# Kernel tuning notes

Measured on AMD Instinct MI355X. Metric: run time of the kernel, lower is better.

Reference implementation:

```python
import jax, jax.numpy as jnp
import numpy as np

B, N, DIM, HEADS, DIM_HEAD = 2, 2048, 1024, 16, 64
INNER = HEADS * DIM_HEAD
LN_EPS = 1e-5


def setup_inputs() -> dict:
    key = jax.random.key(0)
    k1, k2, k3 = jax.random.split(key, 3)
    x = jax.random.normal(k1, (B, N, DIM), dtype=jnp.float32)
    ln_w = jnp.ones((DIM,), dtype=jnp.float32)
    ln_b = jnp.zeros((DIM,), dtype=jnp.float32)
    w_qkv = jax.random.normal(k2, (DIM, 3 * INNER), dtype=jnp.float32) * (DIM ** -0.5)
    w_out = jax.random.normal(k3, (INNER, DIM), dtype=jnp.float32) * (INNER ** -0.5)
    return {"x": x, "ln_w": ln_w, "ln_b": ln_b, "w_qkv": w_qkv, "w_out": w_out}


def reference(x, ln_w, ln_b, w_qkv, w_out):
    scale = DIM_HEAD ** -0.5
    # LayerNorm over last dim
    mu = jnp.mean(x, axis=-1, keepdims=True)
    var = jnp.var(x, axis=-1, keepdims=True)
    xn = (x - mu) / jnp.sqrt(var + LN_EPS) * ln_w + ln_b
    # qkv projection, split, reshape to b h n d
    qkv = xn @ w_qkv  # [B, N, 3*INNER]
    q, k, v = jnp.split(qkv, 3, axis=-1)
    def to_heads(t):
        return t.reshape(B, N, HEADS, DIM_HEAD).transpose(0, 2, 1, 3)
    q, k, v = to_heads(q) * scale, to_heads(k), to_heads(v)
    # scores + causal mask (triu with offset 1 masked)
    sim = jnp.einsum('bhid,bhjd->bhij', q, k)  # [B, H, N, N]
    causal_mask = jnp.triu(jnp.ones((N, N), dtype=bool), k=1)
    sim = jnp.where(causal_mask, -jnp.finfo(sim.dtype).max, sim)
    attn = jax.nn.softmax(sim, axis=-1)
    out = jnp.einsum('bhij,bhjd->bhid', attn, v)  # [B, H, N, D]
    out = out.transpose(0, 2, 1, 3).reshape(B, N, INNER)
    return out @ w_out
```

## Files before the change

### kernel.cpp

```cpp
#include <hip/hip_runtime.h>
#include <stdint.h>

#define BATCH 2
#define NSEQ  2048
#define DIMC  1024
#define NHEAD 16
#define DHEAD 64
#define QKVN  3072
#define MROWS 4096

typedef __attribute__((ext_vector_type(8))) unsigned short u16x8;
typedef __attribute__((ext_vector_type(4))) unsigned short u16x4;
typedef __attribute__((ext_vector_type(8))) short          bf16x8;
typedef __attribute__((ext_vector_type(4))) float          f32x4;

#define F32_PROBE 0x3F800000u
#define QSCALE 0.18033688f

__device__ __forceinline__ float b2f(unsigned short u) {
  union { unsigned int i; float f; } c; c.i = ((unsigned int)u) << 16; return c.f;
}
__device__ __forceinline__ unsigned short f2b(float f) {
  unsigned int u = __float_as_uint(f);
  return (unsigned short)((u + 0x7fffu + ((u >> 16) & 1u)) >> 16);
}
__device__ __forceinline__ float fast_exp2(float x) {
  return __builtin_amdgcn_exp2f(x);
}
__device__ __forceinline__ void async16(const unsigned short* g, unsigned short* s) {
  __builtin_amdgcn_global_load_lds(
      (const __attribute__((address_space(1))) unsigned int*)g,
      (__attribute__((address_space(3))) unsigned int*)s, 16, 0, 0);
}

__device__ __forceinline__ void tr_tile(const void* __restrict__ in,
                                        unsigned short* __restrict__ out,
                                        int R, int C, int r0, int c0, bool f32,
                                        int t, unsigned short (*tile)[33],
                                        int scale_below) {
  int tx = t & 31, ty = t >> 5;
  float sc = (c0 < scale_below) ? QSCALE : 1.0f;
  if (f32) {
    #pragma unroll
    for (int i = 0; i < 32; i += 8)
      tile[ty + i][tx] = f2b(((const float*)in)[(size_t)(r0 + ty + i) * C + c0 + tx] * sc);
  } else {
    #pragma unroll
    for (int i = 0; i < 32; i += 8)
      tile[ty + i][tx] = f2b(b2f(((const unsigned short*)in)[(size_t)(r0 + ty + i) * C + c0 + tx]) * sc);
  }
  __syncthreads();
  #pragma unroll
  for (int i = 0; i < 32; i += 8)
    out[(size_t)(c0 + ty + i) * R + r0 + tx] = tile[tx][ty + i];
}

__global__ __launch_bounds__(256) void prep_kernel(const void* __restrict__ x,
                                                   const void* __restrict__ w,
                                                   const void* __restrict__ bb,
                                                   unsigned short* __restrict__ xn,
                                                   const void* __restrict__ w_qkv,
                                                   unsigned short* __restrict__ wqkvT,
                                                   const void* __restrict__ w_out,
                                                   unsigned short* __restrict__ woutT,
                                                   const unsigned int* __restrict__ probe) {
  __shared__ unsigned short tile[32][33];
  __shared__ float red[8];
  bool f32 = (*probe == F32_PROBE);
  int bid = blockIdx.x, t = threadIdx.x;

  if (bid < MROWS) {
    int row = bid;
    float v0, v1, v2, v3, w0, w1, w2, w3, bb0, bb1, bb2, bb3;
    if (f32) {
      const float* xr = (const float*)x + (size_t)row * DIMC;
      float4 xv = *(const float4*)(xr + t * 4);
      v0 = xv.x; v1 = xv.y; v2 = xv.z; v3 = xv.w;
      float4 wv = *(const float4*)((const float*)w + t * 4);
      w0 = wv.x; w1 = wv.y; w2 = wv.z; w3 = wv.w;
      float4 bv = *(const float4*)((const float*)bb + t * 4);
      bb0 = bv.x; bb1 = bv.y; bb2 = bv.z; bb3 = bv.w;
    } else {
      const unsigned short* xr = (const unsigned short*)x + (size_t)row * DIMC;
      u16x4 xv = *(const u16x4*)(xr + t * 4);
      v0 = b2f(xv[0]); v1 = b2f(xv[1]); v2 = b2f(xv[2]); v3 = b2f(xv[3]);
      u16x4 wv = *(const u16x4*)((const unsigned short*)w + t * 4);
      w0 = b2f(wv[0]); w1 = b2f(wv[1]); w2 = b2f(wv[2]); w3 = b2f(wv[3]);
      u16x4 bv = *(const u16x4*)((const unsigned short*)bb + t * 4);
      bb0 = b2f(bv[0]); bb1 = b2f(bv[1]); bb2 = b2f(bv[2]); bb3 = b2f(bv[3]);
    }
    float s = v0 + v1 + v2 + v3;
    float q = v0 * v0 + v1 * v1 + v2 * v2 + v3 * v3;
    #pragma unroll
    for (int off = 1; off < 64; off <<= 1) { s += __shfl_xor(s, off); q += __shfl_xor(q, off); }
    int wv_ = t >> 6;
    if ((t & 63) == 0) { red[wv_] = s; red[4 + wv_] = q; }
    __syncthreads();
    s = red[0] + red[1] + red[2] + red[3];
    q = red[4] + red[5] + red[6] + red[7];
    float mu  = s * (1.0f / DIMC);
    float var = q * (1.0f / DIMC) - mu * mu;
    float rstd = rsqrtf(var + 1e-5f);
    u16x4 o;
    o[0] = f2b((v0 - mu) * rstd * w0 + bb0);
    o[1] = f2b((v1 - mu) * rstd * w1 + bb1);
    o[2] = f2b((v2 - mu) * rstd * w2 + bb2);
    o[3] = f2b((v3 - mu) * rstd * w3 + bb3);
    *(u16x4*)(xn + (size_t)row * DIMC + t * 4) = o;
  } else if (bid < MROWS + 3072) {
    int tid = bid - MROWS;
    tr_tile(w_qkv, wqkvT, DIMC, QKVN, (tid / 96) * 32, (tid % 96) * 32, f32, t, tile, 1024);
  } else {
    int tid = bid - (MROWS + 3072);
    tr_tile(w_out, woutT, DIMC, DIMC, (tid >> 5) * 32, (tid & 31) * 32, f32, t, tile, 0);
  }
}

__global__ __launch_bounds__(256) void transpose_kernel(const void* __restrict__ in,
                                                        unsigned short* __restrict__ out,
                                                        int R, int C,
                                                        const unsigned int* __restrict__ probe) {
  __shared__ unsigned short tile[32][33];
  bool f32 = (*probe == F32_PROBE);
  int t = threadIdx.x;
  tr_tile(in, out, R, C, blockIdx.y * 32, blockIdx.x * 32, f32, t, tile, 0);
}

__global__ __launch_bounds__(256) void gemm_bt(const unsigned short* __restrict__ A,
                                               const unsigned short* __restrict__ Bt,
                                               void* __restrict__ Cv,
                                               int M, int N, int K, int lda,
                                               int detect_out,
                                               const unsigned int* __restrict__ probe,
                                               unsigned short* __restrict__ vt_out) {
  __shared__ unsigned short As[128 * 32];
  __shared__ unsigned short Bs[128 * 32];
  int t = threadIdx.x;
  int lane = t & 63, wave = t >> 6;
  int l16 = lane & 15, quad = lane >> 4;
  int wm = (wave & 1) * 64, wn = (wave >> 1) * 64;
  int bm = blockIdx.x * 128, bn = blockIdx.y * 128;

  f32x4 acc[4][4] = {};

  int srow = t >> 2;
  int scol = (t & 3) * 8;
  const unsigned short* Ap = A  + (size_t)(bm + srow) * lda + scol;
  const unsigned short* Bp = Bt + (size_t)(bn + srow) * K + scol;
  unsigned short* As0 = &As[srow * 32 + scol];
  unsigned short* As1 = &As[(64 + srow) * 32 + scol];
  unsigned short* Bs0 = &Bs[srow * 32 + scol];
  unsigned short* Bs1 = &Bs[(64 + srow) * 32 + scol];

  for (int k0 = 0; k0 < K; k0 += 32) {
    __syncthreads();
    async16(Ap + k0, As0);
    async16(Ap + (size_t)64 * lda + k0, As1);
    async16(Bp + k0, Bs0);
    async16(Bp + (size_t)64 * K + k0, Bs1);
    __syncthreads();
    bf16x8 af[4], bfr[4];
    #pragma unroll
    for (int mi = 0; mi < 4; mi++)
      af[mi] = *(const bf16x8*)&As[(wm + mi * 16 + l16) * 32 + quad * 8];
    #pragma unroll
    for (int ni = 0; ni < 4; ni++)
      bfr[ni] = *(const bf16x8*)&Bs[(wn + ni * 16 + l16) * 32 + quad * 8];
    #pragma unroll
    for (int mi = 0; mi < 4; mi++)
      #pragma unroll
      for (int ni = 0; ni < 4; ni++)
        acc[mi][ni] = __builtin_amdgcn_mfma_f32_16x16x32_bf16(af[mi], bfr[ni], acc[mi][ni], 0, 0, 0);
  }
  if (vt_out != nullptr && bn >= 2048) {
    #pragma unroll
    for (int mi = 0; mi < 4; mi++)
      #pragma unroll
      for (int ni = 0; ni < 4; ni++) {
        int gc = bn + wn + ni * 16 + l16;
        int hh = (gc >> 6) & 15;
        int dd = gc & 63;
        int gr0 = bm + wm + mi * 16 + quad * 4;
        int bb2 = gr0 >> 11;
        int n0  = gr0 & 2047;
        u16x4 pk;
        #pragma unroll
        for (int r = 0; r < 4; r++) pk[r] = f2b(acc[mi][ni][r]);
        *(u16x4*)&vt_out[(((size_t)(bb2 * 16 + hh) * 64 + dd) << 11) + n0] = pk;
      }
    return;
  }
  bool f32out = detect_out && (*probe == F32_PROBE);
  #pragma unroll
  for (int mi = 0; mi < 4; mi++)
    #pragma unroll
    for (int ni = 0; ni < 4; ni++)
      #pragma unroll
      for (int r = 0; r < 4; r++) {
        int gr = bm + wm + mi * 16 + quad * 4 + r;
        int gc = bn + wn + ni * 16 + l16;
        if (f32out) ((float*)Cv)[(size_t)gr * N + gc] = acc[mi][ni][r];
        else ((unsigned short*)Cv)[(size_t)gr * N + gc] = f2b(acc[mi][ni][r]);
      }
}

__global__ __launch_bounds__(256) void gemm_bt_n64(const unsigned short* __restrict__ A,
                                                   const unsigned short* __restrict__ Bt,
                                                   void* __restrict__ Cv,
                                                   int M, int N, int K, int lda,
                                                   int detect_out,
                                                   const unsigned int* __restrict__ probe) {
  __shared__ unsigned short As[128 * 32];
  __shared__ unsigned short Bs[64 * 32];
  int t = threadIdx.x;
  int lane = t & 63, wave = t >> 6;
  int l16 = lane & 15, quad = lane >> 4;
  int wm = (wave & 1) * 64, wn = (wave >> 1) * 32;
  int bm = blockIdx.x * 128, bn = blockIdx.y * 64;

  f32x4 acc[4][2] = {};

  int srow = t >> 2;
  int scol = (t & 3) * 8;
  const unsigned short* Ap = A  + (size_t)(bm + srow) * lda + scol;
  const unsigned short* Bp = Bt + (size_t)(bn + srow) * K + scol;
  unsigned short* As0 = &As[srow * 32 + scol];
  unsigned short* As1 = &As[(64 + srow) * 32 + scol];
  unsigned short* Bs0 = &Bs[srow * 32 + scol];

  for (int k0 = 0; k0 < K; k0 += 32) {
    __syncthreads();
    async16(Ap + k0, As0);
    async16(Ap + (size_t)64 * lda + k0, As1);
    async16(Bp + k0, Bs0);
    __syncthreads();
    bf16x8 af[4], bfr[2];
    #pragma unroll
    for (int mi = 0; mi < 4; mi++)
      af[mi] = *(const bf16x8*)&As[(wm + mi * 16 + l16) * 32 + quad * 8];
    #pragma unroll
    for (int ni = 0; ni < 2; ni++)
      bfr[ni] = *(const bf16x8*)&Bs[(wn + ni * 16 + l16) * 32 + quad * 8];
    #pragma unroll
    for (int mi = 0; mi < 4; mi++)
      #pragma unroll
      for (int ni = 0; ni < 2; ni++)
        acc[mi][ni] = __builtin_amdgcn_mfma_f32_16x16x32_bf16(af[mi], bfr[ni], acc[mi][ni], 0, 0, 0);
  }
  bool f32out = detect_out && (*probe == F32_PROBE);
  #pragma unroll
  for (int mi = 0; mi < 4; mi++)
    #pragma unroll
    for (int ni = 0; ni < 2; ni++)
      #pragma unroll
      for (int r = 0; r < 4; r++) {
        int gr = bm + wm + mi * 16 + quad * 4 + r;
        int gc = bn + wn + ni * 16 + l16;
        if (f32out) ((float*)Cv)[(size_t)gr * N + gc] = acc[mi][ni][r];
        else ((unsigned short*)Cv)[(size_t)gr * N + gc] = f2b(acc[mi][ni][r]);
      }
}

__device__ __forceinline__ int swz(int row, int chunk) {
  return row * 64 + ((chunk ^ (row & 7)) << 3);
}

__global__ __launch_bounds__(256) void attn_v4(unsigned short* __restrict__ qkv,
                                               const unsigned short* __restrict__ vt) {
  __shared__ unsigned short lds[20480];

  int t = threadIdx.x;
  int lane = t & 63, w = t >> 6;
  int l16 = lane & 15, quad = lane >> 4;
  int pair = blockIdx.x;
  int bh = blockIdx.y;
  int b = bh >> 4, h = bh & 15;
  unsigned short* qbase = qkv + (size_t)(b * NSEQ) * QKVN + h * DHEAD;
  const unsigned short* kbase = qbase + 1024;
  const unsigned short* vtb = vt + (size_t)bh * DHEAD * NSEQ;
  unsigned short* Ps = lds + 16384;

  int sr = t >> 3, sc = t & 7;

  for (int ph = 0; ph < 2; ph++) {
    int qt = ph ? pair : 31 - pair;
    int q0 = qt * 64;

    const unsigned short* qp = qbase + (size_t)(q0 + w * 16 + l16) * QKVN + quad * 8;
    bf16x8 bq0 = *(const bf16x8*)(qp);
    bf16x8 bq1 = *(const bf16x8*)(qp + 32);

    float l_i = 0.f;
    f32x4 o[4] = {};
    u16x8 k0r, k1r, v0r, v1r;

    if (ph) __syncthreads();

    k0r = *(const u16x8*)(kbase + (size_t)sr * QKVN + sc * 8);
    k1r = *(const u16x8*)(kbase + (size_t)(sr + 32) * QKVN + sc * 8);
    v0r = *(const u16x8*)(vtb + (size_t)sr * NSEQ + sc * 8);
    v1r = *(const u16x8*)(vtb + (size_t)(sr + 32) * NSEQ + sc * 8);
    *(u16x8*)&lds[swz(sr, sc)]             = k0r;
    *(u16x8*)&lds[swz(sr + 32, sc)]        = k1r;
    *(u16x8*)&lds[8192 + swz(sr, sc)]      = v0r;
    *(u16x8*)&lds[8192 + swz(sr + 32, sc)] = v1r;
    __syncthreads();

    for (int jt = 0; jt <= qt; jt++) {
      const unsigned short* Kc = lds + (jt & 1) * 4096;
      const unsigned short* Vc = lds + 8192 + (jt & 1) * 4096;

      if (jt < qt) {
        int j0n = (jt + 1) * 64;
        k0r = *(const u16x8*)(kbase + (size_t)(j0n + sr) * QKVN + sc * 8);
        k1r = *(const u16x8*)(kbase + (size_t)(j0n + sr + 32) * QKVN + sc * 8);
        v0r = *(const u16x8*)(vtb + (size_t)sr * NSEQ + j0n + sc * 8);
        v1r = *(const u16x8*)(vtb + (size_t)(sr + 32) * NSEQ + j0n + sc * 8);
      }

      f32x4 s[4];
      #pragma unroll
      for (int mj = 0; mj < 4; mj++)
        #pragma unroll
        for (int r = 0; r < 4; r++) s[mj][r] = -32.0f;
      #pragma unroll
      for (int mj = 0; mj < 4; mj++) {
        bf16x8 ak0 = *(const bf16x8*)&Kc[swz(mj * 16 + l16, quad)];
        s[mj] = __builtin_amdgcn_mfma_f32_16x16x32_bf16(ak0, bq0, s[mj], 0, 0, 0);
        bf16x8 ak1 = *(const bf16x8*)&Kc[swz(mj * 16 + l16, 4 + quad)];
        s[mj] = __builtin_amdgcn_mfma_f32_16x16x32_bf16(ak1, bq1, s[mj], 0, 0, 0);
      }

      if (jt == qt) {
        int il = w * 16 + l16;
        #pragma unroll
        for (int mj = 0; mj < 4; mj++)
          #pragma unroll
          for (int r = 0; r < 4; r++)
            if (mj * 16 + quad * 4 + r > il) s[mj][r] = -1e30f;
      }

      #pragma unroll
      for (int mj = 0; mj < 4; mj++) {
        u16x4 pk;
        #pragma unroll
        for (int r = 0; r < 4; r++) {
          float p = fast_exp2(s[mj][r]);
          l_i += p;
          pk[r] = f2b(p);
        }
        int ch = mj * 2 + (quad >> 1);
        *(u16x4*)&Ps[swz(w * 16 + l16, ch) + (quad & 1) * 4] = pk;
      }

      #pragma unroll
      for (int ks = 0; ks < 2; ks++) {
        bf16x8 ap = *(const bf16x8*)&Ps[swz(w * 16 + l16, ks * 4 + quad)];
        #pragma unroll
        for (int d = 0; d < 4; d++) {
          bf16x8 bv = *(const bf16x8*)&Vc[swz(d * 16 + l16, ks * 4 + quad)];
          o[d] = __builtin_amdgcn_mfma_f32_16x16x32_bf16(ap, bv, o[d], 0, 0, 0);
        }
      }

      if (jt < qt) {
        unsigned short* Kn = lds + ((jt + 1) & 1) * 4096;
        unsigned short* Vn = lds + 8192 + ((jt + 1) & 1) * 4096;
        *(u16x8*)&Kn[swz(sr, sc)]      = k0r;
        *(u16x8*)&Kn[swz(sr + 32, sc)] = k1r;
        *(u16x8*)&Vn[swz(sr, sc)]      = v0r;
        *(u16x8*)&Vn[swz(sr + 32, sc)] = v1r;
        __syncthreads();
      }
    }

    l_i += __shfl_xor(l_i, 16);
    l_i += __shfl_xor(l_i, 32);
    #pragma unroll
    for (int r = 0; r < 4; r++) {
      float lr = __shfl(l_i, (lane & 48) | (quad * 4 + r));
      float inv = 1.0f / lr;
      int row = q0 + w * 16 + quad * 4 + r;
      #pragma unroll
      for (int d = 0; d < 4; d++)
        qbase[(size_t)row * QKVN + d * 16 + l16] = f2b(o[d][r] * inv);
    }
  }
}

extern "C" void kernel_launch(void* const* d_in, const int* in_sizes, int n_in,
                              void* d_out, int out_size, void* d_ws, size_t ws_size,
                              hipStream_t stream) {
  const void* x     = d_in[0];
  const void* ln_w  = d_in[1];
  const void* ln_b  = d_in[2];
  const void* w_qkv = d_in[3];
  const void* w_out = d_in[4];
  const unsigned int* probe = (const unsigned int*)d_in[1];

  unsigned short* wqkvT = (unsigned short*)d_ws;
  unsigned short* qkv   = wqkvT + (size_t)QKVN * DIMC;
  unsigned short* xn    = (unsigned short*)d_out;
  size_t base_e  = (size_t)QKVN * DIMC + (size_t)MROWS * QKVN;
  size_t vt_e    = (size_t)BATCH * NHEAD * DHEAD * NSEQ;
  size_t wout_e  = (size_t)DIMC * DIMC;
  bool fit_vt  = ws_size >= (base_e + vt_e) * 2;
  bool fit_all = ws_size >= (base_e + vt_e + wout_e) * 2;
  unsigned short* vtp   = fit_vt ? qkv + (size_t)MROWS * QKVN
                                 : ((unsigned short*)d_out) + ((size_t)4 * 1024 * 1024);
  unsigned short* woutT = fit_all ? vtp + vt_e : wqkvT;

  int prep_blocks = MROWS + 3072 + (fit_all ? 1024 : 0);
  prep_kernel<<<prep_blocks, 256, 0, stream>>>(x, ln_w, ln_b, xn, w_qkv, wqkvT,
                                               w_out, fit_all ? woutT : nullptr, probe);
  gemm_bt<<<dim3(MROWS / 128, QKVN / 128), 256, 0, stream>>>(
      xn, wqkvT, qkv, MROWS, QKVN, DIMC, DIMC, 0, probe, vtp);
  if (!fit_all)
    transpose_kernel<<<dim3(DIMC / 32, DIMC / 32), 256, 0, stream>>>(w_out, woutT, DIMC, DIMC, probe);
  attn_v4<<<dim3(NSEQ / 128, BATCH * NHEAD), 256, 0, stream>>>(qkv, vtp);
  gemm_bt_n64<<<dim3(MROWS / 128, DIMC / 64), 256, 0, stream>>>(
      qkv, woutT, d_out, MROWS, DIMC, DIMC, QKVN, 1, probe);
}
```

Measured before the change: 186.6 us.

## Replace QKV GEMM with 256x256-tile, 8-wave double-buffered pipelined kernel

The generic 128x128 QKV projection GEMM is replaced by a specialised kernel with 256x256 tiles, 512 threads, and a K-step of 64. It double-buffers the tiles in 128KB of LDS, uses an XOR-swizzled layout to avoid bank conflicts, interleaves async global-to-LDS loads with MFMA quarters, raises wave priority around the MFMA blocks, and swizzles the block order for L2 locality. The aim is to hide memory latency and raise MFMA utilisation in the largest GEMM. In exchange it hardcodes the problem shape and depends on a fragile manual barrier and waitcnt schedule.

```diff
diff --git a/kernel.cpp b/kernel.cpp
--- a/kernel.cpp
+++ b/kernel.cpp
@@ -126,82 +126,137 @@
   tr_tile(in, out, R, C, blockIdx.y * 32, blockIdx.x * 32, f32, t, tile, 0);
 }
 
-__global__ __launch_bounds__(256) void gemm_bt(const unsigned short* __restrict__ A,
-                                               const unsigned short* __restrict__ Bt,
-                                               void* __restrict__ Cv,
-                                               int M, int N, int K, int lda,
-                                               int detect_out,
-                                               const unsigned int* __restrict__ probe,
-                                               unsigned short* __restrict__ vt_out) {
-  __shared__ unsigned short As[128 * 32];
-  __shared__ unsigned short Bs[128 * 32];
+__device__ __forceinline__ void ldA8(bf16x8 (&dst)[8], const unsigned short* base,
+                                     int off, int ch0, int ch1) {
+  #pragma unroll
+  for (int mi = 0; mi < 4; ++mi) {
+    dst[mi * 2 + 0] = *(const bf16x8*)&base[off + mi * 1024 + ch0];
+    dst[mi * 2 + 1] = *(const bf16x8*)&base[off + mi * 1024 + ch1];
+  }
+}
+__device__ __forceinline__ void ldB4(bf16x8 (&dst)[4], const unsigned short* base,
+                                     int off, int ch0, int ch1) {
+  #pragma unroll
+  for (int ni = 0; ni < 2; ++ni) {
+    dst[ni * 2 + 0] = *(const bf16x8*)&base[off + ni * 1024 + ch0];
+    dst[ni * 2 + 1] = *(const bf16x8*)&base[off + ni * 1024 + ch1];
+  }
+}
+__device__ __forceinline__ void mfma16q(f32x4 (&acc)[8][4], const bf16x8 (&a)[8],
+                                        const bf16x8 (&b)[4], int R, int C) {
+  #pragma unroll
+  for (int kh = 0; kh < 2; ++kh)
+    #pragma unroll
+    for (int mi = 0; mi < 4; ++mi)
+      #pragma unroll
+      for (int ni = 0; ni < 2; ++ni)
+        acc[R * 4 + mi][C * 2 + ni] = __builtin_amdgcn_mfma_f32_16x16x32_bf16(
+            a[mi * 2 + kh], b[ni * 2 + kh], acc[R * 4 + mi][C * 2 + ni], 0, 0, 0);
+}
+
+#define SB    asm volatile("s_barrier" ::: "memory")
+#define WVM4  asm volatile("s_waitcnt vmcnt(4)" ::: "memory")
+#define WLG0  asm volatile("s_waitcnt lgkmcnt(0)" ::: "memory")
+#define PRIO1 __builtin_amdgcn_s_setprio(1)
+#define PRIO0 __builtin_amdgcn_s_setprio(0)
+#define STG(gp, g, k0, sb) async16((gp) + (size_t)(g) * 65536 + (k0), (sb) + (g) * 4096 + t8)
+
+__global__ __launch_bounds__(512) void gemm1_8p(const unsigned short* __restrict__ A,
+                                                const unsigned short* __restrict__ Bt,
+                                                unsigned short* __restrict__ C,
+                                                unsigned short* __restrict__ vt_out) {
+  __shared__ unsigned short lds[65536];
+  unsigned short* A0b = lds;
+  unsigned short* B0b = lds + 16384;
+  unsigned short* A1b = lds + 32768;
+  unsigned short* B1b = lds + 49152;
+
   int t = threadIdx.x;
-  int lane = t & 63, wave = t >> 6;
+  int lane = t & 63, wv = t >> 6;
   int l16 = lane & 15, quad = lane >> 4;
-  int wm = (wave & 1) * 64, wn = (wave >> 1) * 64;
-  int bm = blockIdx.x * 128, bn = blockIdx.y * 128;
-
-  f32x4 acc[4][4] = {};
-
-  int srow = t >> 2;
-  int scol = (t & 3) * 8;
-  const unsigned short* Ap = A  + (size_t)(bm + srow) * lda + scol;
-  const unsigned short* Bp = Bt + (size_t)(bn + srow) * K + scol;
-  unsigned short* As0 = &As[srow * 32 + scol];
-  unsigned short* As1 = &As[(64 + srow) * 32 + scol];
-  unsigned short* Bs0 = &Bs[srow * 32 + scol];
-  unsigned short* Bs1 = &Bs[(64 + srow) * 32 + scol];
-
-  for (int k0 = 0; k0 < K; k0 += 32) {
-    __syncthreads();
-    async16(Ap + k0, As0);
-    async16(Ap + (size_t)64 * lda + k0, As1);
-    async16(Bp + k0, Bs0);
-    async16(Bp + (size_t)64 * K + k0, Bs1);
-    __syncthreads();
-    bf16x8 af[4], bfr[4];
-    #pragma unroll
-    for (int mi = 0; mi < 4; mi++)
-      af[mi] = *(const bf16x8*)&As[(wm + mi * 16 + l16) * 32 + quad * 8];
-    #pragma unroll
-    for (int ni = 0; ni < 4; ni++)
-      bfr[ni] = *(const bf16x8*)&Bs[(wn + ni * 16 + l16) * 32 + quad * 8];
-    #pragma unroll
-    for (int mi = 0; mi < 4; mi++)
-      #pragma unroll
-      for (int ni = 0; ni < 4; ni++)
-        acc[mi][ni] = __builtin_amdgcn_mfma_f32_16x16x32_bf16(af[mi], bfr[ni], acc[mi][ni], 0, 0, 0);
-  }
-  if (vt_out != nullptr && bn >= 2048) {
-    #pragma unroll
-    for (int mi = 0; mi < 4; mi++)
-      #pragma unroll
-      for (int ni = 0; ni < 4; ni++) {
-        int gc = bn + wn + ni * 16 + l16;
+  int wr = wv >> 2, wc = wv & 3;
+
+  int bid = blockIdx.x;
+  int swzid = (bid & 7) * 24 + (bid >> 3);
+  int bx = swzid / 12, by = swzid % 12;
+  int bm = bx * 256, bn = by * 256;
+
+  int rl = t >> 3;
+  int sc8 = (((t & 7) ^ (rl & 7)) << 3);
+  int t8 = t * 8;
+  const unsigned short* Ag = A  + (size_t)(bm + rl) * 1024 + sc8;
+  const unsigned short* Bg = Bt + (size_t)(bn + rl) * 1024 + sc8;
+
+  int aoff = (wr * 128 + l16) * 64;
+  int boff = (wc * 64 + l16) * 64;
+  int ch0 = ((quad ^ (l16 & 7)) << 3);
+  int ch1 = (((quad + 4) ^ (l16 & 7)) << 3);
+
+  f32x4 acc[8][4] = {};
+  bf16x8 ar0[8], ar1[8], bc0[4], bc1[4];
+
+  STG(Ag, 0, 0, A0b); STG(Ag, 1, 0, A0b); STG(Ag, 2, 0, A0b); STG(Ag, 3, 0, A0b);
+  STG(Bg, 0, 0, B0b); STG(Bg, 1, 0, B0b); STG(Bg, 2, 0, B0b); STG(Bg, 3, 0, B0b);
+  STG(Ag, 0, 64, A1b); STG(Ag, 1, 64, A1b); STG(Ag, 2, 64, A1b); STG(Ag, 3, 64, A1b);
+  WVM4;
+  SB;
+
+  for (int i = 0; i < 8; ++i) {
+    const int k_b1 = (2 * i + 1) * 64;
+    const int k_n0 = ((2 * i + 2) & 15) * 64;
+    const int k_n1 = ((2 * i + 3) & 15) * 64;
+
+    ldA8(ar0, A0b, aoff, ch0, ch1);
+    ldB4(bc0, B0b, boff, ch0, ch1);
+    STG(Bg, 0, k_b1, B1b); STG(Bg, 1, k_b1, B1b);
+    SB; WLG0; PRIO1; mfma16q(acc, ar0, bc0, 0, 0); PRIO0; SB;
+    ldA8(ar1, A0b, aoff + 4096, ch0, ch1);
+    STG(Bg, 2, k_b1, B1b); STG(Bg, 3, k_b1, B1b);
+    SB; WLG0; PRIO1; mfma16q(acc, ar1, bc0, 1, 0); PRIO0; SB;
+    ldB4(bc1, B0b, boff + 2048, ch0, ch1);
+    STG(Ag, 0, k_n0, A0b); STG(Ag, 1, k_n0, A0b);
+    SB; WLG0; PRIO1; mfma16q(acc, ar0, bc1, 0, 1); PRIO0; SB;
+    STG(Ag, 2, k_n0, A0b); STG(Ag, 3, k_n0, A0b);
+    WVM4;
+    SB; PRIO1; mfma16q(acc, ar1, bc1, 1, 1); PRIO0; SB;
+
+    ldA8(ar0, A1b, aoff, ch0, ch1);
+    ldB4(bc0, B1b, boff, ch0, ch1);
+    STG(Bg, 0, k_n0, B0b); STG(Bg, 1, k_n0, B0b);
+    SB; WLG0; PRIO1; mfma16q(acc, ar0, bc0, 0, 0); PRIO0; SB;
+    ldA8(ar1, A1b, aoff + 4096, ch0, ch1);
+    STG(Bg, 2, k_n0, B0b); STG(Bg, 3, k_n0, B0b);
+    SB; WLG0; PRIO1; mfma16q(acc, ar1, bc0, 1, 0); PRIO0; SB;
+    ldB4(bc1, B1b, boff + 2048, ch0, ch1);
+    STG(Ag, 0, k_n1, A1b); STG(Ag, 1, k_n1, A1b);
+    SB; WLG0; PRIO1; mfma16q(acc, ar0, bc1, 0, 1); PRIO0; SB;
+    STG(Ag, 2, k_n1, A1b); STG(Ag, 3, k_n1, A1b);
+    WVM4;
+    SB; PRIO1; mfma16q(acc, ar1, bc1, 1, 1); PRIO0; SB;
+  }
+
+  bool vblk = (bn >= 2048);
+  #pragma unroll
+  for (int rf = 0; rf < 8; ++rf)
+    #pragma unroll
+    for (int cf = 0; cf < 4; ++cf) {
+      int gr0 = bm + wr * 128 + rf * 16 + quad * 4;
+      int gc  = bn + wc * 64 + cf * 16 + l16;
+      if (vblk) {
         int hh = (gc >> 6) & 15;
         int dd = gc & 63;
-        int gr0 = bm + wm + mi * 16 + quad * 4;
         int bb2 = gr0 >> 11;
         int n0  = gr0 & 2047;
         u16x4 pk;
         #pragma unroll
-        for (int r = 0; r < 4; r++) pk[r] = f2b(acc[mi][ni][r]);
+        for (int r = 0; r < 4; r++) pk[r] = f2b(acc[rf][cf][r]);
         *(u16x4*)&vt_out[(((size_t)(bb2 * 16 + hh) * 64 + dd) << 11) + n0] = pk;
-      }
-    return;
-  }
-  bool f32out = detect_out && (*probe == F32_PROBE);
-  #pragma unroll
-  for (int mi = 0; mi < 4; mi++)
-    #pragma unroll
-    for (int ni = 0; ni < 4; ni++)
-      #pragma unroll
-      for (int r = 0; r < 4; r++) {
-        int gr = bm + wm + mi * 16 + quad * 4 + r;
-        int gc = bn + wn + ni * 16 + l16;
-        if (f32out) ((float*)Cv)[(size_t)gr * N + gc] = acc[mi][ni][r];
-        else ((unsigned short*)Cv)[(size_t)gr * N + gc] = f2b(acc[mi][ni][r]);
-      }
+      } else {
+        #pragma unroll
+        for (int r = 0; r < 4; r++)
+          C[(size_t)(gr0 + r) * QKVN + gc] = f2b(acc[rf][cf][r]);
+      }
+    }
 }
 
 __global__ __launch_bounds__(256) void gemm_bt_n64(const unsigned short* __restrict__ A,
@@ -413,8 +468,7 @@
   int prep_blocks = MROWS + 3072 + (fit_all ? 1024 : 0);
   prep_kernel<<<prep_blocks, 256, 0, stream>>>(x, ln_w, ln_b, xn, w_qkv, wqkvT,
                                                w_out, fit_all ? woutT : nullptr, probe);
-  gemm_bt<<<dim3(MROWS / 128, QKVN / 128), 256, 0, stream>>>(
-      xn, wqkvT, qkv, MROWS, QKVN, DIMC, DIMC, 0, probe, vtp);
+  gemm1_8p<<<dim3(192), 512, 0, stream>>>(xn, wqkvT, qkv, vtp);
   if (!fit_all)
     transpose_kernel<<<dim3(DIMC / 32, DIMC / 32), 256, 0, stream>>>(w_out, woutT, DIMC, DIMC, probe);
   attn_v4<<<dim3(NSEQ / 128, BATCH * NHEAD), 256, 0, stream>>>(qkv, vtp);
```

After: 182.1 us. -2.4%, faster.
